# Optimization experiments

Measured on AMD Instinct MI355X. Metric: run time of the kernel, lower is better.

The kernel has to match this reference:

```python
import jax, jax.numpy as jnp
import numpy as np

N_NODES = 50000
N_EDGES = 800000
D_IN, D_HID, D_OUT = 96, 96, 48


def _gcn_conv(x, src, dst, W, b, num_nodes):
    """PyG GCNConv: h = x @ W; out[dst] += norm * h[src]; out += b.
    Symmetric normalization deg^{-1/2}[src] * deg^{-1/2}[dst], self-loops included
    (src/dst already contain self-loops)."""
    h = x @ W  # [N, d_out]
    deg = jax.ops.segment_sum(jnp.ones_like(dst, dtype=h.dtype), dst,
                              num_segments=num_nodes)  # in-degree incl. self-loop
    dinv = jnp.where(deg > 0, jax.lax.rsqrt(deg), 0.0)
    norm = dinv[src] * dinv[dst]  # [E+N]
    msgs = h[src] * norm[:, None]  # gather + scale (the memory-bound part)
    out = jax.ops.segment_sum(msgs, dst, num_segments=num_nodes)  # scatter-add
    return out + b


def setup_inputs() -> dict:
    key = jax.random.key(0)
    k1, k2, k3, k4 = jax.random.split(key, 4)
    x = jax.random.normal(k1, (N_NODES, D_IN), dtype=jnp.float32)
    edge_index = jax.random.randint(k2, (2, N_EDGES), 0, N_NODES, dtype=jnp.int64)
    # Glorot-ish init for weights, zero bias (matches GCNConv defaults)
    W1 = jax.random.normal(k3, (D_IN, D_HID), dtype=jnp.float32) / np.sqrt(D_IN)
    b1 = jnp.zeros((D_HID,), dtype=jnp.float32)
    W2 = jax.random.normal(k4, (D_HID, D_OUT), dtype=jnp.float32) / np.sqrt(D_HID)
    b2 = jnp.zeros((D_OUT,), dtype=jnp.float32)
    return {"x": x, "edge_index": edge_index, "W1": W1, "b1": b1, "W2": W2, "b2": b2}


def reference(x, edge_index, W1, b1, W2, b2):
    num_nodes = x.shape[0]
    loops = jnp.arange(num_nodes, dtype=edge_index.dtype)
    src = jnp.concatenate([edge_index[0], loops])  # add self-loops
    dst = jnp.concatenate([edge_index[1], loops])
    h = _gcn_conv(x, src, dst, W1, b1, num_nodes)
    h = jax.nn.relu(h)
    # dropout p=0.5 is identity in eval mode (self.training=False)
    out = _gcn_conv(h, src, dst, W2, b2, num_nodes)
    return out
```

## Files before the change

### kernel.cpp

```cpp
#include <hip/hip_runtime.h>
#include <hip/hip_bf16.h>


constexpr int NN = 50000;
constexpr int NE = 800000;
constexpr int DI = 96;
constexpr int DH = 96;
constexpr int DO = 48;

constexpr int BK_SHIFT = 6;
constexpr int NBK      = (NN + 63) >> 6;
constexpr int BK_CAP   = 2048;

constexpr int NCHUNK = 256;
constexpr int CH     = (NE + NCHUNK - 1) / NCHUNK;

typedef unsigned short us8 __attribute__((ext_vector_type(8)));

__device__ __forceinline__ float bf2f(unsigned short u) {
    return __uint_as_float(((unsigned int)u) << 16);
}
__device__ __forceinline__ unsigned short f2bf(float f) {
    __hip_bfloat16 b = __float2bfloat16(f);
    return *reinterpret_cast<unsigned short*>(&b);
}


__global__ __launch_bounds__(256) void k_hist(const int* __restrict__ dst,
                                              int* __restrict__ C, int e) {
    __shared__ int hist[NBK];
    for (int i = threadIdx.x; i < NBK; i += 256) hist[i] = 0;
    __syncthreads();
    const int blk = blockIdx.x;
    const int beg = blk * CH, end = min(beg + CH, e);
    for (int i = beg + threadIdx.x; i < end; i += 256)
        atomicAdd(&hist[dst[i] >> BK_SHIFT], 1);
    __syncthreads();
    for (int b = threadIdx.x; b < NBK; b += 256)
        C[b * NCHUNK + blk] = hist[b];
}

__global__ __launch_bounds__(256) void k_rowscan(int* __restrict__ C,
                                                 int* __restrict__ totals,
                                                 int* __restrict__ row_ptr) {
    if (blockIdx.x == 0 && threadIdx.x == 0) row_ptr[NN] = NE;
    const int w    = threadIdx.x >> 6;
    const int lane = threadIdx.x & 63;
    const int r    = blockIdx.x * 4 + w;
    if (r >= NBK) return;
    int* row = C + r * NCHUNK;
    int v[4], s[4];
#pragma unroll
    for (int q = 0; q < 4; ++q) { v[q] = row[q * 64 + lane]; s[q] = v[q]; }
#pragma unroll
    for (int off = 1; off < 64; off <<= 1) {
#pragma unroll
        for (int q = 0; q < 4; ++q) {
            int y = __shfl_up(s[q], off);
            if (lane >= off) s[q] += y;
        }
    }
    int c0 = __shfl(s[0], 63);
    int c1 = __shfl(s[1], 63);
    int c2 = __shfl(s[2], 63);
    s[1] += c0;
    s[2] += c0 + c1;
    s[3] += c0 + c1 + c2;
#pragma unroll
    for (int q = 0; q < 4; ++q) row[q * 64 + lane] = s[q] - v[q];
    if (lane == 63) totals[r] = s[3];
}

__global__ __launch_bounds__(256) void k_scatter(const int* __restrict__ src,
                                                 const int* __restrict__ dst,
                                                 const int* __restrict__ C,
                                                 const int* __restrict__ totals,
                                                 int* __restrict__ bk_ptr,
                                                 unsigned* __restrict__ ebuf, int e) {
    __shared__ int bkL[NBK + 1];
    __shared__ int part[256];
    __shared__ int cur[NBK];
    const int t = threadIdx.x;

    int v[4];
    int s = 0;
    const int base = t * 4;
#pragma unroll
    for (int i = 0; i < 4; ++i) {
        int idx = base + i;
        v[i] = (idx < NBK) ? totals[idx] : 0;
        s += v[i];
    }
    part[t] = s;
    __syncthreads();
#pragma unroll
    for (int off = 1; off < 256; off <<= 1) {
        int x = part[t];
        int a = (t >= off) ? part[t - off] : 0;
        __syncthreads();
        part[t] = x + a;
        __syncthreads();
    }
    int run = part[t] - s;
#pragma unroll
    for (int i = 0; i < 4; ++i) {
        int idx = base + i;
        if (idx <= NBK) bkL[idx] = run;
        run += v[i];
    }
    __syncthreads();

    const int blk = blockIdx.x;
    for (int b = t; b < NBK; b += 256) cur[b] = bkL[b] + C[b * NCHUNK + blk];
    if (blk == 0)
        for (int i = t; i <= NBK; i += 256) bk_ptr[i] = bkL[i];
    __syncthreads();

    const int beg = blk * CH, end = min(beg + CH, e);
    for (int i = beg + t; i < end; i += 256) {
        int d = dst[i];
        int b = d >> BK_SHIFT;
        int pos = atomicAdd(&cur[b], 1);
        ebuf[pos] = ((unsigned)(d & 63) << 16) | (unsigned)src[i];
    }
}

__global__ __launch_bounds__(256) void k_bsort(const unsigned* __restrict__ ebuf,
                                               const int* __restrict__ bk_ptr,
                                               int* __restrict__ row_ptr,
                                               float* __restrict__ dinv,
                                               unsigned short* __restrict__ src16, int n) {
    __shared__ unsigned eL[BK_CAP];
    __shared__ unsigned short outL[BK_CAP];
    __shared__ int curL[64];
    __shared__ int baseL[64];

    const int b   = blockIdx.x;
    const int beg = bk_ptr[b];
    const int m   = bk_ptr[b + 1] - beg;
    const int t   = threadIdx.x;

    if (t < 64) curL[t] = 0;
    __syncthreads();

    for (int i = t; i < m; i += 256) {
        unsigned v = ebuf[beg + i];
        eL[i] = v;
        atomicAdd(&curL[v >> 16], 1);
    }
    __syncthreads();

    if (t < 64) {
        int c = curL[t];
        int x = c;
#pragma unroll
        for (int off = 1; off < 64; off <<= 1) {
            int y = __shfl_up(x, off);
            if (t >= off) x += y;
        }
        int excl = x - c;
        baseL[t] = excl;
        int d0 = (b << BK_SHIFT) + t;
        if (d0 < n) {
            row_ptr[d0] = beg + excl;
            dinv[d0]    = rsqrtf((float)(c + 1));
        }
    }
    __syncthreads();
    if (t < 64) curL[t] = baseL[t];
    __syncthreads();

    for (int i = t; i < m; i += 256) {
        unsigned v = eL[i];
        int p = atomicAdd(&curL[v >> 16], 1);
        outL[p] = (unsigned short)(v & 0xFFFFu);
    }
    __syncthreads();
    for (int i = t; i < m; i += 256) src16[beg + i] = outL[i];
}


template<int DOUT, bool XBF16>
__global__ __launch_bounds__(256) void k_gemm(const void* __restrict__ Xin,
                                              const float* __restrict__ W,
                                              const float* __restrict__ dinv,
                                              unsigned short* __restrict__ H, int n) {
    constexpr int ROWS = 32;
    constexpr int CPT  = DOUT / 16;
    constexpr int RPT  = 2;

    __shared__ float ws[DI * DOUT];
    __shared__ unsigned char xraw[ROWS * DI * (XBF16 ? 2 : 4)];
    float*          xsf = reinterpret_cast<float*>(xraw);
    unsigned short* xsu = reinterpret_cast<unsigned short*>(xraw);

    const int tid  = threadIdx.x;
    const int row0 = blockIdx.x * ROWS;

    for (int i = tid; i < DI * DOUT; i += 256) ws[i] = W[i];

    if (XBF16) {
        const us8* Xv = reinterpret_cast<const us8*>(
            (const unsigned short*)Xin + (size_t)row0 * DI);
        us8* xv = reinterpret_cast<us8*>(xsu);
        const int nv   = ROWS * DI / 8;
        const int maxv = ((n - row0) * DI) / 8;
        for (int i = tid; i < nv; i += 256)
            xv[i] = (i < maxv) ? Xv[i] : (us8)(0);
    } else {
        const float4* Xv = reinterpret_cast<const float4*>(
            (const float*)Xin + (size_t)row0 * DI);
        float4* xv = reinterpret_cast<float4*>(xsf);
        const int nv   = ROWS * DI / 4;
        const int maxv = ((n - row0) * DI) / 4;
        for (int i = tid; i < nv; i += 256)
            xv[i] = (i < maxv) ? Xv[i] : float4{0.f, 0.f, 0.f, 0.f};
    }
    __syncthreads();

    const int cg = tid & 15;
    const int rg = tid >> 4;

    float acc[RPT][CPT];
#pragma unroll
    for (int i = 0; i < RPT; ++i)
#pragma unroll
        for (int j = 0; j < CPT; ++j) acc[i][j] = 0.f;

    for (int k = 0; k < DI; ++k) {
        float xv[RPT];
#pragma unroll
        for (int i = 0; i < RPT; ++i) {
            int r = rg * RPT + i;
            xv[i] = XBF16 ? bf2f(xsu[r * DI + k]) : xsf[r * DI + k];
        }
#pragma unroll
        for (int j = 0; j < CPT; ++j) {
            float wv = ws[k * DOUT + cg * CPT + j];
#pragma unroll
            for (int i = 0; i < RPT; ++i) acc[i][j] += xv[i] * wv;
        }
    }

#pragma unroll
    for (int i = 0; i < RPT; ++i) {
        int row = row0 + rg * RPT + i;
        if (row < n) {
            float dv = dinv[row];
#pragma unroll
            for (int j = 0; j < CPT; ++j)
                H[(size_t)row * DOUT + cg * CPT + j] = f2bf(acc[i][j] * dv);
        }
    }
}


template<int D, bool RELU, bool OUTBF16>
__global__ __launch_bounds__(256) void k_agg_csr(const unsigned short* __restrict__ h,
                                                 const float* __restrict__ dinv,
                                                 const int* __restrict__ row_ptr,
                                                 const unsigned short* __restrict__ src16,
                                                 const float* __restrict__ bias,
                                                 void* __restrict__ outp, int n) {
    constexpr int G = D / 8;
    int t = blockIdx.x * blockDim.x + threadIdx.x;
    if (t >= n * G) return;
    const int node = t / G;
    const int g    = t % G;

    const us8* h8 = reinterpret_cast<const us8*>(h);

    float accA[8], accB[8];
    {
        us8 hv = h8[(size_t)node * G + g];
#pragma unroll
        for (int j = 0; j < 8; ++j) { accA[j] = bf2f(hv[j]); accB[j] = 0.f; }
    }

    const int beg = row_ptr[node];
    const int end = row_ptr[node + 1];
    int k = beg;
    int kA = min((beg + 7) & ~7, end);
    for (; k < kA; ++k) {
        us8 vv = h8[(size_t)src16[k] * G + g];
#pragma unroll
        for (int j = 0; j < 8; ++j) accA[j] += bf2f(vv[j]);
    }
    for (; k + 8 <= end; k += 8) {
        us8 si = *reinterpret_cast<const us8*>(src16 + k);
        us8 v0 = h8[(size_t)si[0] * G + g];
        us8 v1 = h8[(size_t)si[1] * G + g];
        us8 v2 = h8[(size_t)si[2] * G + g];
        us8 v3 = h8[(size_t)si[3] * G + g];
        us8 v4 = h8[(size_t)si[4] * G + g];
        us8 v5 = h8[(size_t)si[5] * G + g];
        us8 v6 = h8[(size_t)si[6] * G + g];
        us8 v7 = h8[(size_t)si[7] * G + g];
#pragma unroll
        for (int j = 0; j < 8; ++j) {
            accA[j] += (bf2f(v0[j]) + bf2f(v1[j])) + (bf2f(v4[j]) + bf2f(v5[j]));
            accB[j] += (bf2f(v2[j]) + bf2f(v3[j])) + (bf2f(v6[j]) + bf2f(v7[j]));
        }
    }
    for (; k < end; ++k) {
        us8 vv = h8[(size_t)src16[k] * G + g];
#pragma unroll
        for (int j = 0; j < 8; ++j) accB[j] += bf2f(vv[j]);
    }

    const float di = dinv[node];
    const float4* b4 = reinterpret_cast<const float4*>(bias);
    float4 b0 = b4[g * 2], b1 = b4[g * 2 + 1];
    float r[8];
#pragma unroll
    for (int j = 0; j < 8; ++j) r[j] = di * (accA[j] + accB[j]);
    r[0] += b0.x; r[1] += b0.y; r[2] += b0.z; r[3] += b0.w;
    r[4] += b1.x; r[5] += b1.y; r[6] += b1.z; r[7] += b1.w;
    if (RELU) {
#pragma unroll
        for (int j = 0; j < 8; ++j) r[j] = fmaxf(r[j], 0.f);
    }
    if (OUTBF16) {
        us8 o;
#pragma unroll
        for (int j = 0; j < 8; ++j) o[j] = f2bf(r[j]);
        reinterpret_cast<us8*>((unsigned short*)outp)[(size_t)node * G + g] = o;
    } else {
        float4* o4 = reinterpret_cast<float4*>((float*)outp + (size_t)node * D + g * 8);
        o4[0] = float4{r[0], r[1], r[2], r[3]};
        o4[1] = float4{r[4], r[5], r[6], r[7]};
    }
}


extern "C" void kernel_launch(void* const* d_in, const int* in_sizes, int n_in,
                              void* d_out, int out_size, void* d_ws, size_t ws_size,
                              hipStream_t stream) {
    const float* x   = (const float*)d_in[0];
    const int*   ei  = (const int*)d_in[1];
    const float* W1  = (const float*)d_in[2];
    const float* b1  = (const float*)d_in[3];
    const float* W2  = (const float*)d_in[4];
    const float* b2  = (const float*)d_in[5];
    float*       out = (float*)d_out;

    const int* srcv = ei;
    const int* dstv = ei + NE;

    char* p = (char*)d_ws;
    float*          dinv  = (float*)p;           p += (size_t)NN * 4;
    unsigned short* a1    = (unsigned short*)p;  p += (size_t)NN * DH * 2;
    unsigned short* h1    = (unsigned short*)p;  p += (size_t)NN * DH * 2;
    int*      row_ptr     = (int*)p;             p += (size_t)(NN + 16) * 4;
    unsigned short* src16 = (unsigned short*)p;  p += (size_t)NE * 2;
    unsigned* ebuf        = (unsigned*)p;        p += (size_t)NE * 4;
    int*      Cm          = (int*)p;             p += (size_t)NBK * NCHUNK * 4;
    int*      totals      = (int*)p;             p += (size_t)NBK * 4;
    int*      bk_ptr      = (int*)p;             p += (size_t)(NBK + 1) * 4;

    const int B = 256;

    k_hist<<<NCHUNK, B, 0, stream>>>(dstv, Cm, NE);
    k_rowscan<<<(NBK + 3) / 4, B, 0, stream>>>(Cm, totals, row_ptr);
    k_scatter<<<NCHUNK, B, 0, stream>>>(srcv, dstv, Cm, totals, bk_ptr, ebuf, NE);
    k_bsort<<<NBK, B, 0, stream>>>(ebuf, bk_ptr, row_ptr, dinv, src16, NN);

    k_gemm<DH, false><<<(NN + 31) / 32, B, 0, stream>>>(x, W1, dinv, h1, NN);
    {
        int total = NN * (DH / 8);
        k_agg_csr<DH, true, true><<<(total + B - 1) / B, B, 0, stream>>>(
            h1, dinv, row_ptr, src16, b1, a1, NN);
    }

    unsigned short* h2 = h1;
    k_gemm<DO, true><<<(NN + 31) / 32, B, 0, stream>>>(a1, W2, dinv, h2, NN);
    {
        int total = NN * (DO / 8);
        k_agg_csr<DO, false, false><<<(total + B - 1) / B, B, 0, stream>>>(
            h2, dinv, row_ptr, src16, b2, out, NN);
    }
}
```

Before: 123.9 us.

## Slice layer-1 features into 32-column planes and aggregate per slice

The first GEMM now writes its bf16 output as three separate 32-column slabs. A new aggregation kernel gathers from one slab at a time, using blockIdx to interleave slices and node ranges, with 8-wide unrolled neighbor gathers. The aim is to shrink the gather working set per slice so it fits better in cache during the random-access aggregation. Both GEMMs also move to 64-row tiles with padded shared memory and 4x6 or 4x3 register blocking. The slice mapping relies on hard-coded constants, with 3 slices and a split of 2-3 reps, which adds complexity.

```diff
diff --git a/kernel.cpp b/kernel.cpp
--- a/kernel.cpp
+++ b/kernel.cpp
@@ -180,78 +180,195 @@
 }
 
 
-template<int DOUT, bool XBF16>
-__global__ __launch_bounds__(256) void k_gemm(const void* __restrict__ Xin,
-                                              const float* __restrict__ W,
-                                              const float* __restrict__ dinv,
-                                              unsigned short* __restrict__ H, int n) {
-    constexpr int ROWS = 32;
-    constexpr int CPT  = DOUT / 16;
-    constexpr int RPT  = 2;
-
-    __shared__ float ws[DI * DOUT];
-    __shared__ unsigned char xraw[ROWS * DI * (XBF16 ? 2 : 4)];
-    float*          xsf = reinterpret_cast<float*>(xraw);
-    unsigned short* xsu = reinterpret_cast<unsigned short*>(xraw);
+__global__ __launch_bounds__(256) void k_gemm1(const float* __restrict__ X,
+                                               const float* __restrict__ W,
+                                               const float* __restrict__ dinv,
+                                               unsigned short* __restrict__ Hsl, int n) {
+    constexpr int ROWS = 64, P = 97;
+    __shared__ float ws[DI * DH];
+    __shared__ float xs[ROWS * P];
+    unsigned short* hout = reinterpret_cast<unsigned short*>(xs);
 
     const int tid  = threadIdx.x;
     const int row0 = blockIdx.x * ROWS;
 
-    for (int i = tid; i < DI * DOUT; i += 256) ws[i] = W[i];
-
-    if (XBF16) {
-        const us8* Xv = reinterpret_cast<const us8*>(
-            (const unsigned short*)Xin + (size_t)row0 * DI);
-        us8* xv = reinterpret_cast<us8*>(xsu);
-        const int nv   = ROWS * DI / 8;
-        const int maxv = ((n - row0) * DI) / 8;
-        for (int i = tid; i < nv; i += 256)
-            xv[i] = (i < maxv) ? Xv[i] : (us8)(0);
-    } else {
-        const float4* Xv = reinterpret_cast<const float4*>(
-            (const float*)Xin + (size_t)row0 * DI);
-        float4* xv = reinterpret_cast<float4*>(xsf);
+    for (int i = tid; i < DI * DH; i += 256) ws[i] = W[i];
+    {
+        const float4* Xv = reinterpret_cast<const float4*>(X + (size_t)row0 * DI);
         const int nv   = ROWS * DI / 4;
         const int maxv = ((n - row0) * DI) / 4;
-        for (int i = tid; i < nv; i += 256)
-            xv[i] = (i < maxv) ? Xv[i] : float4{0.f, 0.f, 0.f, 0.f};
-    }
-    __syncthreads();
-
-    const int cg = tid & 15;
-    const int rg = tid >> 4;
-
-    float acc[RPT][CPT];
-#pragma unroll
-    for (int i = 0; i < RPT; ++i)
-#pragma unroll
-        for (int j = 0; j < CPT; ++j) acc[i][j] = 0.f;
-
+        for (int i = tid; i < nv; i += 256) {
+            float4 v = (i < maxv) ? Xv[i] : float4{0.f, 0.f, 0.f, 0.f};
+            int r = i / 24, c = (i % 24) * 4;
+            xs[r * P + c + 0] = v.x;
+            xs[r * P + c + 1] = v.y;
+            xs[r * P + c + 2] = v.z;
+            xs[r * P + c + 3] = v.w;
+        }
+    }
+    __syncthreads();
+
+    const int cg = tid & 15, rg = tid >> 4;
+    float acc[4][6] = {};
+#pragma unroll 2
     for (int k = 0; k < DI; ++k) {
-        float xv[RPT];
-#pragma unroll
-        for (int i = 0; i < RPT; ++i) {
-            int r = rg * RPT + i;
-            xv[i] = XBF16 ? bf2f(xsu[r * DI + k]) : xsf[r * DI + k];
-        }
-#pragma unroll
-        for (int j = 0; j < CPT; ++j) {
-            float wv = ws[k * DOUT + cg * CPT + j];
-#pragma unroll
-            for (int i = 0; i < RPT; ++i) acc[i][j] += xv[i] * wv;
-        }
-    }
-
-#pragma unroll
-    for (int i = 0; i < RPT; ++i) {
-        int row = row0 + rg * RPT + i;
+        float xv[4];
+#pragma unroll
+        for (int i = 0; i < 4; ++i) xv[i] = xs[(rg * 4 + i) * P + k];
+#pragma unroll
+        for (int j = 0; j < 6; ++j) {
+            float wv = ws[k * DH + cg * 6 + j];
+#pragma unroll
+            for (int i = 0; i < 4; ++i) acc[i][j] += xv[i] * wv;
+        }
+    }
+    __syncthreads();
+
+#pragma unroll
+    for (int i = 0; i < 4; ++i) {
+        int row = row0 + rg * 4 + i;
+        float dv = (row < n) ? dinv[row] : 0.f;
+#pragma unroll
+        for (int j = 0; j < 6; ++j)
+            hout[(rg * 4 + i) * 96 + cg * 6 + j] = f2bf(acc[i][j] * dv);
+    }
+    __syncthreads();
+
+    if (tid < 192) {
+        int s = tid >> 6, r = tid & 63;
+        int row = row0 + r;
+        if (row < n) {
+            const us8* srcp = reinterpret_cast<const us8*>(hout + r * 96 + s * 32);
+            us8* dstp = reinterpret_cast<us8*>(Hsl + ((size_t)s * n + row) * 32);
+#pragma unroll
+            for (int q = 0; q < 4; ++q) dstp[q] = srcp[q];
+        }
+    }
+}
+
+
+__global__ __launch_bounds__(256) void k_gemm2(const unsigned short* __restrict__ A,
+                                               const float* __restrict__ W,
+                                               const float* __restrict__ dinv,
+                                               unsigned short* __restrict__ H, int n) {
+    constexpr int ROWS = 64, P = 98;
+    __shared__ float ws[DH * DO];
+    __shared__ unsigned short xs[ROWS * P];
+
+    const int tid  = threadIdx.x;
+    const int row0 = blockIdx.x * ROWS;
+
+    for (int i = tid; i < DH * DO; i += 256) ws[i] = W[i];
+    {
+        const us8* Av = reinterpret_cast<const us8*>(A + (size_t)row0 * DH);
+        const int nv   = ROWS * DH / 8;
+        const int maxv = ((n - row0) * DH) / 8;
+        for (int i = tid; i < nv; i += 256) {
+            us8 v = (i < maxv) ? Av[i] : (us8)(0);
+            int r = i / 12, c = (i % 12) * 8;
+#pragma unroll
+            for (int jj = 0; jj < 8; ++jj) xs[r * P + c + jj] = v[jj];
+        }
+    }
+    __syncthreads();
+
+    const int cg = tid & 15, rg = tid >> 4;
+    float acc[4][3] = {};
+#pragma unroll 2
+    for (int k = 0; k < DH; ++k) {
+        float xv[4];
+#pragma unroll
+        for (int i = 0; i < 4; ++i) xv[i] = bf2f(xs[(rg * 4 + i) * P + k]);
+#pragma unroll
+        for (int j = 0; j < 3; ++j) {
+            float wv = ws[k * DO + cg * 3 + j];
+#pragma unroll
+            for (int i = 0; i < 4; ++i) acc[i][j] += xv[i] * wv;
+        }
+    }
+
+#pragma unroll
+    for (int i = 0; i < 4; ++i) {
+        int row = row0 + rg * 4 + i;
         if (row < n) {
             float dv = dinv[row];
 #pragma unroll
-            for (int j = 0; j < CPT; ++j)
-                H[(size_t)row * DOUT + cg * CPT + j] = f2bf(acc[i][j] * dv);
-        }
-    }
+            for (int j = 0; j < 3; ++j)
+                H[(size_t)row * DO + cg * 3 + j] = f2bf(acc[i][j] * dv);
+        }
+    }
+}
+
+
+__global__ __launch_bounds__(256) void k_agg_sl3(const unsigned short* __restrict__ hsl,
+                                                 const float* __restrict__ dinv,
+                                                 const int* __restrict__ row_ptr,
+                                                 const unsigned short* __restrict__ src16,
+                                                 const float* __restrict__ bias,
+                                                 unsigned short* __restrict__ a1, int n) {
+    const int v   = blockIdx.x & 7;
+    const int s   = (v >= 6) ? (v - 6) : (v >= 3 ? v - 3 : v);
+    const int rep = (v >= 6) ? 2 : (v >= 3 ? 1 : 0);
+    const int R   = (s == 2) ? 2 : 3;
+    const int cnt = (n + R - 1) / R;
+    const int lo  = rep * cnt;
+    const int hi  = min(lo + cnt, n);
+    const int node = lo + ((int)(blockIdx.x >> 3) << 6) + ((int)threadIdx.x >> 2);
+    if (node >= hi) return;
+    const int g = threadIdx.x & 3;
+
+    const us8* hs = reinterpret_cast<const us8*>(hsl + (size_t)s * n * 32);
+
+    float accA[8], accB[8];
+    {
+        us8 hv = hs[(size_t)node * 4 + g];
+#pragma unroll
+        for (int j = 0; j < 8; ++j) { accA[j] = bf2f(hv[j]); accB[j] = 0.f; }
+    }
+
+    const int beg = row_ptr[node];
+    const int end = row_ptr[node + 1];
+    int k = beg;
+    int kA = min((beg + 7) & ~7, end);
+    for (; k < kA; ++k) {
+        us8 vv = hs[(size_t)src16[k] * 4 + g];
+#pragma unroll
+        for (int j = 0; j < 8; ++j) accA[j] += bf2f(vv[j]);
+    }
+    for (; k + 8 <= end; k += 8) {
+        us8 si = *reinterpret_cast<const us8*>(src16 + k);
+        us8 v0 = hs[(size_t)si[0] * 4 + g];
+        us8 v1 = hs[(size_t)si[1] * 4 + g];
+        us8 v2 = hs[(size_t)si[2] * 4 + g];
+        us8 v3 = hs[(size_t)si[3] * 4 + g];
+        us8 v4 = hs[(size_t)si[4] * 4 + g];
+        us8 v5 = hs[(size_t)si[5] * 4 + g];
+        us8 v6 = hs[(size_t)si[6] * 4 + g];
+        us8 v7 = hs[(size_t)si[7] * 4 + g];
+#pragma unroll
+        for (int j = 0; j < 8; ++j) {
+            accA[j] += (bf2f(v0[j]) + bf2f(v1[j])) + (bf2f(v4[j]) + bf2f(v5[j]));
+            accB[j] += (bf2f(v2[j]) + bf2f(v3[j])) + (bf2f(v6[j]) + bf2f(v7[j]));
+        }
+    }
+    for (; k < end; ++k) {
+        us8 vv = hs[(size_t)src16[k] * 4 + g];
+#pragma unroll
+        for (int j = 0; j < 8; ++j) accB[j] += bf2f(vv[j]);
+    }
+
+    const float di = dinv[node];
+    const float4* b4 = reinterpret_cast<const float4*>(bias);
+    float4 b0 = b4[s * 8 + g * 2], b1 = b4[s * 8 + g * 2 + 1];
+    float r[8];
+#pragma unroll
+    for (int j = 0; j < 8; ++j) r[j] = di * (accA[j] + accB[j]);
+    r[0] += b0.x; r[1] += b0.y; r[2] += b0.z; r[3] += b0.w;
+    r[4] += b1.x; r[5] += b1.y; r[6] += b1.z; r[7] += b1.w;
+    us8 o;
+#pragma unroll
+    for (int j = 0; j < 8; ++j) o[j] = f2bf(fmaxf(r[j], 0.f));
+    *reinterpret_cast<us8*>(a1 + (size_t)node * DH + s * 32 + g * 8) = o;
 }
 
 
@@ -350,7 +467,7 @@
     char* p = (char*)d_ws;
     float*          dinv  = (float*)p;           p += (size_t)NN * 4;
     unsigned short* a1    = (unsigned short*)p;  p += (size_t)NN * DH * 2;
-    unsigned short* h1    = (unsigned short*)p;  p += (size_t)NN * DH * 2;
+    unsigned short* h1sl  = (unsigned short*)p;  p += (size_t)3 * NN * 32 * 2;
     int*      row_ptr     = (int*)p;             p += (size_t)(NN + 16) * 4;
     unsigned short* src16 = (unsigned short*)p;  p += (size_t)NE * 2;
     unsigned* ebuf        = (unsigned*)p;        p += (size_t)NE * 4;
@@ -365,15 +482,14 @@
     k_scatter<<<NCHUNK, B, 0, stream>>>(srcv, dstv, Cm, totals, bk_ptr, ebuf, NE);
     k_bsort<<<NBK, B, 0, stream>>>(ebuf, bk_ptr, row_ptr, dinv, src16, NN);
 
-    k_gemm<DH, false><<<(NN + 31) / 32, B, 0, stream>>>(x, W1, dinv, h1, NN);
-    {
-        int total = NN * (DH / 8);
-        k_agg_csr<DH, true, true><<<(total + B - 1) / B, B, 0, stream>>>(
-            h1, dinv, row_ptr, src16, b1, a1, NN);
-    }
-
-    unsigned short* h2 = h1;
-    k_gemm<DO, true><<<(NN + 31) / 32, B, 0, stream>>>(a1, W2, dinv, h2, NN);
+    k_gemm1<<<(NN + 63) / 64, B, 0, stream>>>(x, W1, dinv, h1sl, NN);
+    {
+        const int NCH = ((NN + 1) / 2 + 63) / 64;
+        k_agg_sl3<<<NCH * 8, B, 0, stream>>>(h1sl, dinv, row_ptr, src16, b1, a1, NN);
+    }
+
+    unsigned short* h2 = h1sl;
+    k_gemm2<<<(NN + 63) / 64, B, 0, stream>>>(a1, W2, dinv, h2, NN);
     {
         int total = NN * (DO / 8);
         k_agg_csr<DO, false, false><<<(total + B - 1) / B, B, 0, stream>>>(
```

Result: slower. 132.6 us (+7.0%).
